# Kernel tuning notes

Measured on AMD Instinct MI355X. Metric: run time of the kernel, lower is better.

## Reference

```python
import jax, jax.numpy as jnp
import numpy as np

jax.config.update("jax_enable_x64", True)

B, T, D, L, H = 128, 256, 64, 64, 256   # batch, time steps, phys dim, latent dim, hidden width
P, DT = 4, 1.0                          # num_pred_steps, delta_t


def _mlp(x, ws, bs):
    # Conv1D(kernel_size=1) stack == per-timestep dense; relu hidden, linear output
    for i, (W, b) in enumerate(zip(ws, bs)):
        x = x @ W + b
        if i < len(ws) - 1:
            x = jax.nn.relu(x)
    return x


def setup_inputs() -> dict:
    key = jax.random.key(0)
    ks = jax.random.split(key, 9)

    def glorot(k, fi, fo):
        return jax.random.normal(k, (fi, fo), jnp.float64) * np.sqrt(2.0 / (fi + fo))

    inp = {"x": jax.random.normal(ks[0], (B, T, D), jnp.float64)}
    enc_dims = [(D, H), (H, H), (H, H), (H, L)]
    dec_dims = [(L, H), (H, H), (H, H), (H, D)]
    for i, (fi, fo) in enumerate(enc_dims):
        inp[f"enc_w{i}"] = glorot(ks[1 + i], fi, fo)
        inp[f"enc_b{i}"] = jnp.zeros((fo,), jnp.float64)
    for i, (fi, fo) in enumerate(dec_dims):
        inp[f"dec_w{i}"] = glorot(ks[5 + i], fi, fo)
        inp[f"dec_b{i}"] = jnp.zeros((fo,), jnp.float64)
    return inp


def _edmd(y, x):
    # y: [B, L, T] latent trajectories, x: [B, D, T] physical trajectories (D == L)
    y_m, y_p = y[:, :, :-1], y[:, :, 1:]
    # full_matrices=True followed by slicing to r=min(L,T-1)=L cols == reduced SVD
    U, S, Vh = jnp.linalg.svd(y_m, full_matrices=False)
    V = jnp.swapaxes(Vh, -1, -2)
    pinv = (V / S[:, None, :]) @ jnp.swapaxes(U, -1, -2)   # V @ diag(1/S) @ U^H
    K = y_p @ pinv                                         # [B, L, L]
    evals, modes = jnp.linalg.eig(K)                       # complex128
    k_evals = jnp.log(evals) / DT                          # [B, L]
    k_efuns = jnp.linalg.solve(modes, x.astype(modes.dtype))  # [B, L, T]
    xint = k_efuns[:, :, -1:]                              # [B, L, 1]

    # repeated squaring of diag eigenvalue matrix, one matvec per prediction step
    def step(e, _):
        yp = (modes @ (e[:, :, None] * xint))[..., 0]      # [B, L]
        return e * e, yp

    _, ys = jax.lax.scan(step, k_evals * k_evals, None, length=P)
    y_pred = jnp.transpose(ys, (1, 0, 2))                  # [B, P, L]
    return k_efuns, k_evals, modes, y_pred


def reference(x, enc_w0, enc_b0, enc_w1, enc_b1, enc_w2, enc_b2, enc_w3, enc_b3,
              dec_w0, dec_b0, dec_w1, dec_b1, dec_w2, dec_b2, dec_w3, dec_b3):
    ews = [enc_w0, enc_w1, enc_w2, enc_w3]
    ebs = [enc_b0, enc_b1, enc_b2, enc_b3]
    dws = [dec_w0, dec_w1, dec_w2, dec_w3]
    dbs = [dec_b0, dec_b1, dec_b2, dec_b3]

    y = _mlp(x, ews, ebs)        # [B, T, L]
    x_ae = _mlp(y, dws, dbs)     # [B, T, D]

    yt = jnp.swapaxes(y, 1, 2)   # [B, L, T]
    xt = jnp.swapaxes(x, 1, 2)   # [B, D, T]
    k_efuns, k_evals, k_modes, y_adv = _edmd(yt, xt)
    y_adv_real = jnp.real(y_adv)
    y_adv_imag = jnp.imag(y_adv)
    x_adv = _mlp(y_adv_real, dws, dbs)  # [B, P, D]
    return y, x_ae, x_adv, y_adv_real, y_adv_imag, k_evals, k_efuns, k_modes
```

## Files before the change

kernel.cpp:

```cpp
#include <hip/hip_runtime.h>
#include <hip/hip_bf16.h>

#define NB 128
#define NT 256
#define ND 64
#define NL 64
#define NH 256
#define NP 4

__device__ double g_ws[3145728];

static __device__ __forceinline__ double dlapy2_(double x, double y) {
  double ax = fabs(x), ay = fabs(y);
  double w = ax > ay ? ax : ay;
  double z = ax > ay ? ay : ax;
  if (z == 0.0) return w;
  double r = z / w;
  return w * sqrt(1.0 + r * r);
}
static __device__ __forceinline__ double sgn1_(double x) { return copysign(1.0, x); }
static __device__ __forceinline__ void cdiv_(double ar, double ai, double br, double bi,
                                             double& cr, double& ci) {
  if (fabs(br) >= fabs(bi)) {
    double r = bi / br, den = br + r * bi;
    cr = (ar + ai * r) / den;
    ci = (ai - ar * r) / den;
  } else {
    double r = br / bi, den = bi + r * br;
    cr = (ar * r + ai) / den;
    ci = (ai * r - ar) / den;
  }
}
static __device__ __forceinline__ void fwg(float* out, long long ofs, long long lim,
                                           double v) {
  if (ofs >= 0 && ofs < lim) out[ofs] = (float)v;
}
static __device__ __forceinline__ double wsum_(double v) {
  for (int o = 32; o > 0; o >>= 1) v += __shfl_xor(v, o, 64);
  return v;
}
static __device__ __forceinline__ double wmax_(double v) {
  for (int o = 32; o > 0; o >>= 1) v = fmax(v, __shfl_xor(v, o, 64));
  return v;
}

static __device__ void dlanv2_(double& a, double& b, double& c, double& d,
                               double& rt1r, double& rt1i, double& rt2r, double& rt2i,
                               double& cs, double& sn) {
  const double eps = 2.2204460492503131e-16;
  if (c == 0.0) {
    cs = 1.0; sn = 0.0;
  } else if (b == 0.0) {
    cs = 0.0; sn = 1.0;
    double temp = d; d = a; a = temp;
    b = -c; c = 0.0;
  } else if ((a - d) == 0.0 && sgn1_(b) != sgn1_(c)) {
    cs = 1.0; sn = 0.0;
  } else {
    double temp = a - d;
    double p = 0.5 * temp;
    double bcmax = fmax(fabs(b), fabs(c));
    double bcmis = fmin(fabs(b), fabs(c)) * sgn1_(b) * sgn1_(c);
    double scale = fmax(fabs(p), bcmax);
    double z = (p / scale) * p + (bcmax / scale) * bcmis;
    if (z >= 4.0 * eps) {
      z = p + copysign(sqrt(scale) * sqrt(z), p);
      a = d + z;
      d = d - (bcmax / z) * bcmis;
      double tau = dlapy2_(c, z);
      cs = z / tau; sn = c / tau;
      b = b - c; c = 0.0;
    } else {
      double sigma = b + c;
      double tau = dlapy2_(sigma, temp);
      cs = sqrt(0.5 * (1.0 + fabs(sigma) / tau));
      sn = -(p / (tau * cs)) * sgn1_(sigma);
      double aa = a * cs + b * sn, bb = -a * sn + b * cs;
      double cc = c * cs + d * sn, dd = -c * sn + d * cs;
      a = aa * cs + cc * sn; b = bb * cs + dd * sn;
      c = -aa * sn + cc * cs; d = -bb * sn + dd * cs;
      temp = 0.5 * (a + d);
      a = temp; d = temp;
      if (c != 0.0) {
        if (b != 0.0) {
          if (sgn1_(b) == sgn1_(c)) {
            double sab = sqrt(fabs(b)), sac = sqrt(fabs(c));
            double p2 = copysign(sab * sac, c);
            double tau2 = 1.0 / sqrt(fabs(b + c));
            a = temp + p2; d = temp - p2;
            b = b - c; c = 0.0;
            double cs1 = sab * tau2, sn1 = sac * tau2;
            double t0 = cs * cs1 - sn * sn1;
            sn = cs * sn1 + sn * cs1;
            cs = t0;
          }
        } else {
          b = -c; c = 0.0;
          double t0 = cs; cs = -sn; sn = t0;
        }
      }
    }
  }
  rt1r = a; rt2r = d;
  if (c == 0.0) { rt1i = 0.0; rt2i = 0.0; }
  else { rt1i = sqrt(fabs(b)) * sqrt(fabs(c)); rt2i = -rt1i; }
}

__global__ __launch_bounds__(256) void encdec_kernel(
    const float* __restrict__ x,
    const float* __restrict__ EW0, const float* __restrict__ EB0,
    const float* __restrict__ EW1, const float* __restrict__ EB1,
    const float* __restrict__ EW2, const float* __restrict__ EB2,
    const float* __restrict__ EW3, const float* __restrict__ EB3,
    const float* __restrict__ DW0, const float* __restrict__ DB0,
    const float* __restrict__ DW1, const float* __restrict__ DB1,
    const float* __restrict__ DW2, const float* __restrict__ DB2,
    const float* __restrict__ DW3, const float* __restrict__ DB3,
    float* __restrict__ out_y, double* __restrict__ y64,
    float* __restrict__ out_xae, long long lim)
{
  const int tid = threadIdx.x;
  const long long tok0 = (long long)blockIdx.x * 8;
  __shared__ double xin[8][64];
  __shared__ double h0[8][256];
  __shared__ double h1[8][256];
  for (int idx = tid; idx < 512; idx += 256) {
    int tk = idx >> 6, f2 = idx & 63;
    xin[tk][f2] = (double)x[(tok0 + tk) * 64 + f2];
  }
  __syncthreads();
  {
    int j = tid; double acc[8]; double bj = (double)EB0[j];
    for (int tk = 0; tk < 8; ++tk) acc[tk] = bj;
#pragma unroll 8
    for (int i2 = 0; i2 < 64; ++i2) {
      double w = (double)EW0[i2 * 256 + j];
      for (int tk = 0; tk < 8; ++tk) acc[tk] += xin[tk][i2] * w;
    }
    for (int tk = 0; tk < 8; ++tk) h0[tk][j] = fmax(acc[tk], 0.0);
  }
  __syncthreads();
  {
    int j = tid; double acc[8]; double bj = (double)EB1[j];
    for (int tk = 0; tk < 8; ++tk) acc[tk] = bj;
#pragma unroll 4
    for (int i2 = 0; i2 < 256; ++i2) {
      double w = (double)EW1[i2 * 256 + j];
      for (int tk = 0; tk < 8; ++tk) acc[tk] += h0[tk][i2] * w;
    }
    for (int tk = 0; tk < 8; ++tk) h1[tk][j] = fmax(acc[tk], 0.0);
  }
  __syncthreads();
  {
    int j = tid; double acc[8]; double bj = (double)EB2[j];
    for (int tk = 0; tk < 8; ++tk) acc[tk] = bj;
#pragma unroll 4
    for (int i2 = 0; i2 < 256; ++i2) {
      double w = (double)EW2[i2 * 256 + j];
      for (int tk = 0; tk < 8; ++tk) acc[tk] += h1[tk][i2] * w;
    }
    for (int tk = 0; tk < 8; ++tk) h0[tk][j] = fmax(acc[tk], 0.0);
  }
  __syncthreads();
  {
    int j = tid & 63;
    int tg = tid >> 6;
    double acc0 = (double)EB3[j], acc1 = acc0;
#pragma unroll 4
    for (int i2 = 0; i2 < 256; ++i2) {
      double w = (double)EW3[i2 * 64 + j];
      acc0 += h0[tg * 2][i2] * w;
      acc1 += h0[tg * 2 + 1][i2] * w;
    }
    for (int u = 0; u < 2; ++u) {
      int tk = tg * 2 + u;
      double a = (u == 0) ? acc0 : acc1;
      long long gl = (tok0 + tk) * 64 + j;
      xin[tk][j] = a;
      fwg(out_y, gl, lim, a);
      y64[gl] = a;
    }
  }
  __syncthreads();
  {
    int j = tid; double acc[8]; double bj = (double)DB0[j];
    for (int tk = 0; tk < 8; ++tk) acc[tk] = bj;
#pragma unroll 8
    for (int i2 = 0; i2 < 64; ++i2) {
      double w = (double)DW0[i2 * 256 + j];
      for (int tk = 0; tk < 8; ++tk) acc[tk] += xin[tk][i2] * w;
    }
    for (int tk = 0; tk < 8; ++tk) h0[tk][j] = fmax(acc[tk], 0.0);
  }
  __syncthreads();
  {
    int j = tid; double acc[8]; double bj = (double)DB1[j];
    for (int tk = 0; tk < 8; ++tk) acc[tk] = bj;
#pragma unroll 4
    for (int i2 = 0; i2 < 256; ++i2) {
      double w = (double)DW1[i2 * 256 + j];
      for (int tk = 0; tk < 8; ++tk) acc[tk] += h0[tk][i2] * w;
    }
    for (int tk = 0; tk < 8; ++tk) h1[tk][j] = fmax(acc[tk], 0.0);
  }
  __syncthreads();
  {
    int j = tid; double acc[8]; double bj = (double)DB2[j];
    for (int tk = 0; tk < 8; ++tk) acc[tk] = bj;
#pragma unroll 4
    for (int i2 = 0; i2 < 256; ++i2) {
      double w = (double)DW2[i2 * 256 + j];
      for (int tk = 0; tk < 8; ++tk) acc[tk] += h1[tk][i2] * w;
    }
    for (int tk = 0; tk < 8; ++tk) h0[tk][j] = fmax(acc[tk], 0.0);
  }
  __syncthreads();
  {
    int j = tid & 63;
    int tg = tid >> 6;
    double acc0 = (double)DB3[j], acc1 = acc0;
#pragma unroll 4
    for (int i2 = 0; i2 < 256; ++i2) {
      double w = (double)DW3[i2 * 64 + j];
      acc0 += h0[tg * 2][i2] * w;
      acc1 += h0[tg * 2 + 1][i2] * w;
    }
    fwg(out_xae, (tok0 + tg * 2) * 64 + j, lim, acc0);
    fwg(out_xae, (tok0 + tg * 2 + 1) * 64 + j, lim, acc1);
  }
}

__global__ __launch_bounds__(256) void dec4_kernel(
    const double* __restrict__ inp, long long ntok,
    const float* __restrict__ W0, const float* __restrict__ B0,
    const float* __restrict__ W1, const float* __restrict__ B1,
    const float* __restrict__ W2, const float* __restrict__ B2,
    const float* __restrict__ W3, const float* __restrict__ B3,
    float* __restrict__ outb, long long lim)
{
  const int tid = threadIdx.x;
  const long long tok0 = (long long)blockIdx.x * 8;
  __shared__ double xin[8][64];
  __shared__ double h0[8][256];
  __shared__ double h1[8][256];
  for (int idx = tid; idx < 512; idx += 256) {
    int tk = idx >> 6, f2 = idx & 63;
    long long gl = (tok0 + tk) * 64 + f2;
    xin[tk][f2] = (tok0 + tk < ntok) ? inp[gl] : 0.0;
  }
  __syncthreads();
  {
    int j = tid; double acc[8]; double bj = (double)B0[j];
    for (int tk = 0; tk < 8; ++tk) acc[tk] = bj;
#pragma unroll 8
    for (int i2 = 0; i2 < 64; ++i2) {
      double w = (double)W0[i2 * 256 + j];
      for (int tk = 0; tk < 8; ++tk) acc[tk] += xin[tk][i2] * w;
    }
    for (int tk = 0; tk < 8; ++tk) h0[tk][j] = fmax(acc[tk], 0.0);
  }
  __syncthreads();
  {
    int j = tid; double acc[8]; double bj = (double)B1[j];
    for (int tk = 0; tk < 8; ++tk) acc[tk] = bj;
#pragma unroll 4
    for (int i2 = 0; i2 < 256; ++i2) {
      double w = (double)W1[i2 * 256 + j];
      for (int tk = 0; tk < 8; ++tk) acc[tk] += h0[tk][i2] * w;
    }
    for (int tk = 0; tk < 8; ++tk) h1[tk][j] = fmax(acc[tk], 0.0);
  }
  __syncthreads();
  {
    int j = tid; double acc[8]; double bj = (double)B2[j];
    for (int tk = 0; tk < 8; ++tk) acc[tk] = bj;
#pragma unroll 4
    for (int i2 = 0; i2 < 256; ++i2) {
      double w = (double)W2[i2 * 256 + j];
      for (int tk = 0; tk < 8; ++tk) acc[tk] += h1[tk][i2] * w;
    }
    for (int tk = 0; tk < 8; ++tk) h0[tk][j] = fmax(acc[tk], 0.0);
  }
  __syncthreads();
  {
    int j = tid & 63;
    int tg = tid >> 6;
    double acc0 = (double)B3[j], acc1 = acc0;
#pragma unroll 4
    for (int i2 = 0; i2 < 256; ++i2) {
      double w = (double)W3[i2 * 64 + j];
      acc0 += h0[tg * 2][i2] * w;
      acc1 += h0[tg * 2 + 1][i2] * w;
    }
    for (int u = 0; u < 2; ++u) {
      long long tok = tok0 + tg * 2 + u;
      if (tok < ntok) fwg(outb, tok * 64 + j, lim, (u == 0) ? acc0 : acc1);
    }
  }
}

__global__ __launch_bounds__(256) void buildGA_kernel(const double* __restrict__ y64,
                                                      double* __restrict__ G,
                                                      double* __restrict__ A)
{
  int b = blockIdx.x, tid = threadIdx.x;
  __shared__ double ybuf[65][64];
  const double* yb = y64 + (size_t)b * NT * 64;
  double g[16], a[16];
  for (int s = 0; s < 16; ++s) { g[s] = 0.0; a[s] = 0.0; }
  for (int c0 = 0; c0 < 255; c0 += 64) {
    int nrow = (256 - c0 < 65) ? (256 - c0) : 65;
    for (int idx = tid; idx < nrow * 64; idx += 256) {
      int rr = idx >> 6, f2 = idx & 63;
      ybuf[rr][f2] = yb[(size_t)(c0 + rr) * 64 + f2];
    }
    __syncthreads();
    int tmax = (254 - c0 < 63) ? (254 - c0) : 63;
    for (int s = 0; s < 16; ++s) {
      int id = s * 256 + tid;
      int i2 = id >> 6, j2 = id & 63;
      double gg = g[s], aa = a[s];
      for (int tt = 0; tt <= tmax; ++tt) {
        double yj = ybuf[tt][j2];
        gg += ybuf[tt][i2] * yj;
        aa += ybuf[tt + 1][i2] * yj;
      }
      g[s] = gg; a[s] = aa;
    }
    __syncthreads();
  }
  for (int s = 0; s < 16; ++s) {
    int id = s * 256 + tid;
    G[(size_t)b * 4096 + id] = g[s];
    A[(size_t)b * 4096 + id] = a[s];
  }
}

__global__ __launch_bounds__(64) void cholsolve_kernel(const double* __restrict__ G,
                                                       const double* __restrict__ A,
                                                       double* __restrict__ Km)
{
  int b = blockIdx.x, t = threadIdx.x;
  __shared__ double C[64][65];
  __shared__ double X[64][65];
  const double* Gb = G + (size_t)b * 4096;
  const double* Ab = A + (size_t)b * 4096;
  for (int r = 0; r < 64; ++r) C[r][t] = Gb[r * 64 + t];
  for (int i2 = 0; i2 < 64; ++i2) X[i2][t] = Ab[t * 64 + i2];
  __syncthreads();
  for (int k = 0; k < 64; ++k) {
    double s = C[k][k];
    for (int m2 = 0; m2 < k; ++m2) s -= C[k][m2] * C[k][m2];
    double ckk = sqrt(fmax(s, 1e-300));
    __syncthreads();
    if (t == k) C[k][k] = ckk;
    if (t > k) {
      double v = C[t][k];
      for (int m2 = 0; m2 < k; ++m2) v -= C[t][m2] * C[k][m2];
      C[t][k] = v / ckk;
    }
    __syncthreads();
  }
  for (int i2 = 0; i2 < 64; ++i2) {
    double v = X[i2][t];
    for (int m2 = 0; m2 < i2; ++m2) v -= C[i2][m2] * X[m2][t];
    X[i2][t] = v / C[i2][i2];
  }
  for (int i2 = 63; i2 >= 0; --i2) {
    double v = X[i2][t];
    for (int m2 = i2 + 1; m2 < 64; ++m2) v -= C[m2][i2] * X[m2][t];
    X[i2][t] = v / C[i2][i2];
  }
  __syncthreads();
  for (int i2 = 0; i2 < 64; ++i2)
    Km[(size_t)b * 4096 + (size_t)t * 64 + i2] = X[i2][t];
}

__global__ __launch_bounds__(64) void eig_kernel(
    const double* __restrict__ Kmat,
    double* __restrict__ modes_re, double* __restrict__ modes_im,
    double* __restrict__ klog,
    float* __restrict__ out, long long o_kevals, long long o_kmodes,
    int cplx, long long lim)
{
  const int b = blockIdx.x;
  const int t = threadIdx.x;
  __shared__ double Hs[64][65];
  __shared__ double Zs[64][65];
  __shared__ double wr[64], wi[64], bscale[64], tau[64];
  __shared__ double xr[64], xi[64];
  double* mre = modes_re + (size_t)b * 4096;
  double* mim = modes_im + (size_t)b * 4096;

  const double ulp = 2.2204460492503131e-16;
  const double safmin = 2.2250738585072014e-308;

  for (int r = 0; r < 64; ++r) Hs[r][t] = Kmat[(size_t)b * 4096 + r * 64 + t];
  bscale[t] = 1.0;
  __syncthreads();

  {
    const double sclfac = 2.0, factor = 0.95;
    const double sfmin1 = safmin / ulp;
    const double sfmax1 = 1.0 / sfmin1;
    const double sfmin2 = sfmin1 * sclfac;
    const double sfmax2 = 1.0 / sfmin2;
    for (int sweep = 0; sweep < 64; ++sweep) {
      bool noconv = false;
      for (int i = 0; i < 64; ++i) {
        double colv = fabs(Hs[t][i]);
        double rowv = fabs(Hs[i][t]);
        double c = wsum_((t == i) ? 0.0 : colv);
        double r = wsum_((t == i) ? 0.0 : rowv);
        double ca = wmax_(colv);
        double ra = wmax_(rowv);
        if (c == 0.0 || r == 0.0) continue;
        double g = r / sclfac, f = 1.0, s = c + r;
        while (c < g) {
          if (fmax(fmax(f, c), ca) >= sfmax2 || fmin(fmin(r, g), ra) <= sfmin2) break;
          f *= sclfac; c *= sclfac; ca *= sclfac;
          r /= sclfac; g /= sclfac; ra /= sclfac;
        }
        g = c / sclfac;
        while (g >= r) {
          if (fmax(r, ra) >= sfmax2 || fmin(fmin(fmin(f, c), g), ca) <= sfmin2) break;
          f /= sclfac; c /= sclfac; g /= sclfac; ca /= sclfac;
          r *= sclfac; ra *= sclfac;
        }
        if (c + r >= factor * s) continue;
        double bsi = bscale[i];
        if (f < 1.0 && bsi < 1.0) { if (f * bsi <= sfmin1) continue; }
        if (f > 1.0 && bsi > 1.0) { if (bsi >= sfmax1 / f) continue; }
        double gi = 1.0 / f;
        Hs[i][t] *= gi;
        Hs[t][i] *= f;
        if (t == 0) bscale[i] = bsi * f;
        noconv = true;
        __syncthreads();
      }
      if (!noconv) break;
    }
    __syncthreads();
  }

  for (int i = 0; i < 62; ++i) {
    double alpha = Hs[i + 1][i];
    double contrib = (t >= i + 2) ? Hs[t][i] * Hs[t][i] : 0.0;
    double ss = wsum_(contrib);
    double taui, beta;
    if (ss == 0.0) {
      taui = 0.0; beta = alpha;
    } else {
      beta = -copysign(sqrt(alpha * alpha + ss), alpha);
      taui = (beta - alpha) / beta;
      double sc = 1.0 / (alpha - beta);
      if (t >= i + 2) Hs[t][i] *= sc;
    }
    if (t == 0) { tau[i] = taui; Hs[i + 1][i] = beta; }
    __syncthreads();
    if (taui != 0.0) {
      {
        double sum = Hs[t][i + 1];
        for (int k = i + 2; k < 64; ++k) sum += Hs[t][k] * Hs[k][i];
        sum *= taui;
        Hs[t][i + 1] -= sum;
        for (int k = i + 2; k < 64; ++k) Hs[t][k] -= sum * Hs[k][i];
      }
      __syncthreads();
      if (t >= i + 1) {
        double sum = Hs[i + 1][t];
        for (int k = i + 2; k < 64; ++k) sum += Hs[k][i] * Hs[k][t];
        sum *= taui;
        Hs[i + 1][t] -= sum;
        for (int k = i + 2; k < 64; ++k) Hs[k][t] -= sum * Hs[k][i];
      }
      __syncthreads();
    }
  }

  {
    for (int r = 0; r < 64; ++r) Zs[t][r] = (r == t) ? 1.0 : 0.0;
    for (int i = 61; i >= 0; --i) {
      double taui = tau[i];
      if (taui != 0.0) {
        double sum = Zs[t][i + 1];
        for (int k = i + 2; k < 64; ++k) sum += Hs[k][i] * Zs[t][k];
        sum *= taui;
        Zs[t][i + 1] -= sum;
        for (int k = i + 2; k < 64; ++k) Zs[t][k] -= sum * Hs[k][i];
      }
    }
  }
  __syncthreads();
  for (int r = t + 2; r < 64; ++r) Hs[r][t] = 0.0;
  __syncthreads();

  {
    const int lo = 0, hi = 63;
    const double dat1 = 0.75, dat2 = -0.4375;
    const int kexsh = 10;
    const double smlnum = safmin * (64.0 / ulp);
    int I = hi;
    int kdefl = 0;
    while (I >= lo) {
      int L = lo;
      bool done = false;
      const int itmax = 30 * 64;
      for (int its = 0; its <= itmax; ++its) {
        int k;
        {
          bool pred = false;
          int kl = t;
          if (kl > L && kl <= I) {
            double sub = fabs(Hs[kl][kl - 1]);
            if (sub <= smlnum) pred = true;
            else {
              double tst = fabs(Hs[kl - 1][kl - 1]) + fabs(Hs[kl][kl]);
              if (tst == 0.0) {
                if (kl - 2 >= lo) tst += fabs(Hs[kl - 1][kl - 2]);
                if (kl + 1 <= hi) tst += fabs(Hs[kl + 1][kl]);
              }
              if (sub <= ulp * tst) {
                double h12a = fabs(Hs[kl - 1][kl]);
                double ab = fmax(sub, h12a), ba = fmin(sub, h12a);
                double hkk = fabs(Hs[kl][kl]);
                double dif = fabs(Hs[kl - 1][kl - 1] - Hs[kl][kl]);
                double aa = fmax(hkk, dif), bb2 = fmin(hkk, dif);
                double s = aa + ab;
                if (ba * (ab / s) <= fmax(smlnum, ulp * (bb2 * (aa / s)))) pred = true;
              }
            }
          }
          unsigned long long msk = __ballot(pred);
          k = msk ? (63 - __builtin_clzll(msk)) : L;
        }
        L = k;
        if (L > lo) { if (t == 0) Hs[L][L - 1] = 0.0; }
        __syncthreads();
        if (L >= I - 1) { done = true; break; }
        kdefl++;
        double h11, h12, h21, h22;
        if (kdefl % (2 * kexsh) == 0) {
          double s = dat1 * (fabs(Hs[I][I - 1]) + fabs(Hs[I - 1][I - 2]));
          h11 = dat2 * s + Hs[I][I]; h12 = s; h21 = s; h22 = h11;
        } else if (kdefl % kexsh == 0) {
          double s = dat1 * (fabs(Hs[L + 1][L]) + fabs(Hs[L + 2][L + 1]));
          h11 = dat2 * s + Hs[L][L]; h12 = s; h21 = s; h22 = h11;
        } else {
          h11 = Hs[I - 1][I - 1]; h21 = Hs[I][I - 1];
          h12 = Hs[I - 1][I];     h22 = Hs[I][I];
        }
        double rt1r, rt1i, rt2r, rt2i;
        {
          double s = fabs(h11) + fabs(h12) + fabs(h21) + fabs(h22);
          if (s == 0.0) { rt1r = rt1i = rt2r = rt2i = 0.0; }
          else {
            double a_ = h11 / s, c_ = h21 / s, b_ = h12 / s, d_ = h22 / s;
            double tr = a_ + d_;
            double det = (a_ - d_) * (a_ - d_) * 0.25 + b_ * c_;
            if (det >= 0.0) {
              double rtdisc = sqrt(det);
              double r1 = tr * 0.5 + rtdisc;
              double r2 = tr * 0.5 - rtdisc;
              double pick = (fabs(r1 - d_) <= fabs(r2 - d_)) ? r1 : r2;
              rt1r = pick * s; rt2r = rt1r; rt1i = 0.0; rt2i = 0.0;
            } else {
              rt1r = tr * 0.5 * s; rt2r = rt1r;
              rt1i = sqrt(-det) * s; rt2i = -rt1i;
            }
          }
        }
        int m; double v0, v1, v2;
        {
          double w0 = 0.0, w1 = 0.0, w2 = 0.0;
          bool ok = false;
          int mm = t;
          if (mm >= L && mm <= I - 2) {
            double h21s = Hs[mm + 1][mm];
            double s = fabs(Hs[mm][mm] - rt2r) + fabs(rt2i) + fabs(h21s);
            h21s = Hs[mm + 1][mm] / s;
            w0 = h21s * Hs[mm][mm + 1] + (Hs[mm][mm] - rt1r) * ((Hs[mm][mm] - rt2r) / s)
                 - rt1i * (rt2i / s);
            w1 = h21s * (Hs[mm][mm] + Hs[mm + 1][mm + 1] - rt1r - rt2r);
            w2 = h21s * Hs[mm + 2][mm + 1];
            double s2 = fabs(w0) + fabs(w1) + fabs(w2);
            w0 /= s2; w1 /= s2; w2 /= s2;
            if (mm == L) ok = true;
            else ok = (fabs(Hs[mm][mm - 1]) * (fabs(w1) + fabs(w2)) <=
                       ulp * fabs(w0) *
                           (fabs(Hs[mm - 1][mm - 1]) + fabs(Hs[mm][mm]) +
                            fabs(Hs[mm + 1][mm + 1])));
          }
          unsigned long long msk = __ballot(ok);
          m = 63 - __builtin_clzll(msk);
          v0 = __shfl(w0, m); v1 = __shfl(w1, m); v2 = __shfl(w2, m);
        }
        for (int kk = m; kk <= I - 1; ++kk) {
          int nr = (3 < I - kk + 1) ? 3 : (I - kk + 1);
          double u0, u1, u2 = 0.0;
          if (kk > m) {
            u0 = Hs[kk][kk - 1]; u1 = Hs[kk + 1][kk - 1];
            u2 = (nr == 3) ? Hs[kk + 2][kk - 1] : 0.0;
          } else { u0 = v0; u1 = v1; u2 = (nr == 3) ? v2 : 0.0; }
          double t1;
          {
            double xn2 = u1 * u1 + u2 * u2;
            if (xn2 == 0.0) t1 = 0.0;
            else {
              double beta = -copysign(sqrt(u0 * u0 + xn2), u0);
              t1 = (beta - u0) / beta;
              double sc = 1.0 / (u0 - beta);
              u1 *= sc; u2 *= sc;
              u0 = beta;
            }
          }
          double t2 = t1 * u1, t3 = t1 * u2;
          if (nr == 3) {
            if (t >= kk) {
              double sum = Hs[kk][t] + u1 * Hs[kk + 1][t] + u2 * Hs[kk + 2][t];
              Hs[kk][t] -= sum * t1;
              Hs[kk + 1][t] -= sum * t2;
              Hs[kk + 2][t] -= sum * t3;
            }
          } else {
            if (t >= kk) {
              double sum = Hs[kk][t] + u1 * Hs[kk + 1][t];
              Hs[kk][t] -= sum * t1;
              Hs[kk + 1][t] -= sum * t2;
            }
          }
          if (t == 0) {
            if (kk > m) {
              Hs[kk][kk - 1] = u0;
              Hs[kk + 1][kk - 1] = 0.0;
              if (kk < I - 1) Hs[kk + 2][kk - 1] = 0.0;
            } else if (m > L) {
              Hs[kk][kk - 1] *= (1.0 - t1);
            }
          }
          __syncthreads();
          int rmax = (kk + 3 < I) ? kk + 3 : I;
          if (nr == 3) {
            if (t <= rmax) {
              double sum = Hs[t][kk] + u1 * Hs[t][kk + 1] + u2 * Hs[t][kk + 2];
              Hs[t][kk] -= sum * t1;
              Hs[t][kk + 1] -= sum * t2;
              Hs[t][kk + 2] -= sum * t3;
            }
            {
              double z0 = Zs[kk][t], z1 = Zs[kk + 1][t], z2 = Zs[kk + 2][t];
              double sum = z0 + u1 * z1 + u2 * z2;
              Zs[kk][t] = z0 - sum * t1;
              Zs[kk + 1][t] = z1 - sum * t2;
              Zs[kk + 2][t] = z2 - sum * t3;
            }
          } else {
            if (t <= rmax) {
              double sum = Hs[t][kk] + u1 * Hs[t][kk + 1];
              Hs[t][kk] -= sum * t1;
              Hs[t][kk + 1] -= sum * t2;
            }
            {
              double z0 = Zs[kk][t], z1 = Zs[kk + 1][t];
              double sum = z0 + u1 * z1;
              Zs[kk][t] = z0 - sum * t1;
              Zs[kk + 1][t] = z1 - sum * t2;
            }
          }
          __syncthreads();
        }
      }
      if (!done) {
        __syncthreads();
        if (t == 0) {
          for (int r = lo; r <= I; ++r) { wr[r] = Hs[r][r]; wi[r] = 0.0; }
        }
        __syncthreads();
        I = lo - 1;
        kdefl = 0;
        continue;
      }
      if (L == I) {
        if (t == 0) { wr[I] = Hs[I][I]; wi[I] = 0.0; }
        __syncthreads();
      } else {
        double a_ = Hs[I - 1][I - 1], b_ = Hs[I - 1][I];
        double c_ = Hs[I][I - 1],     d_ = Hs[I][I];
        double r1r, r1i, r2r, r2i, cs, sn;
        dlanv2_(a_, b_, c_, d_, r1r, r1i, r2r, r2i, cs, sn);
        __syncthreads();
        if (t == 0) {
          Hs[I - 1][I - 1] = a_; Hs[I - 1][I] = b_;
          Hs[I][I - 1] = c_;     Hs[I][I] = d_;
          wr[I - 1] = r1r; wi[I - 1] = r1i;
          wr[I] = r2r;     wi[I] = r2i;
        }
        __syncthreads();
        if (t > I) {
          double x = Hs[I - 1][t], y = Hs[I][t];
          Hs[I - 1][t] = cs * x + sn * y;
          Hs[I][t] = cs * y - sn * x;
        }
        if (t < I - 1) {
          double x = Hs[t][I - 1], y = Hs[t][I];
          Hs[t][I - 1] = cs * x + sn * y;
          Hs[t][I] = cs * y - sn * x;
        }
        {
          double x = Zs[I - 1][t], y = Zs[I][t];
          Zs[I - 1][t] = cs * x + sn * y;
          Zs[I][t] = cs * y - sn * x;
        }
        __syncthreads();
      }
      kdefl = 0;
      I = L - 1;
    }
  }
  __syncthreads();

  const double smln = safmin * (64.0 / ulp);
  int ki = 63;
  while (ki >= 0) {
    bool pair = (ki > 0) && (Hs[ki][ki - 1] != 0.0);
    if (!pair) {
      double lam = wr[ki];
      double smin = fmax(ulp * fabs(lam), smln);
      xr[t] = (t < ki) ? -Hs[t][ki] : ((t == ki) ? 1.0 : 0.0);
      __syncthreads();
      int j = ki - 1;
      while (j >= 0) {
        bool blk2 = (j > 0) && (Hs[j][j - 1] != 0.0);
        if (!blk2) {
          double den = Hs[j][j] - lam;
          if (fabs(den) < smin) den = smin;
          double xj = xr[j] / den;
          if (t == j) xr[j] = xj;
          else if (t < j) xr[t] -= xj * Hs[t][j];
          __syncthreads();
          j -= 1;
        } else {
          double t11 = Hs[j - 1][j - 1] - lam, t12 = Hs[j - 1][j];
          double t21 = Hs[j][j - 1], t22 = Hs[j][j] - lam;
          double det = t11 * t22 - t12 * t21;
          if (fabs(det) < smin * smin) det = copysign(smin * smin, (det == 0.0) ? 1.0 : det);
          double b1 = xr[j - 1], b2 = xr[j];
          double x1 = (b1 * t22 - t12 * b2) / det;
          double x2 = (t11 * b2 - t21 * b1) / det;
          if (t == j - 1) xr[j - 1] = x1;
          else if (t == j) xr[j] = x2;
          else if (t < j - 1) xr[t] -= x1 * Hs[t][j - 1] + x2 * Hs[t][j];
          __syncthreads();
          j -= 2;
        }
      }
      double acc = 0.0;
      for (int k2 = 0; k2 <= ki; ++k2) acc += Zs[k2][t] * xr[k2];
      acc *= bscale[t];
      double nn = wsum_(acc * acc);
      double scl = 1.0 / sqrt(nn);
      mre[t * 64 + ki] = acc * scl;
      mim[t * 64 + ki] = 0.0;
      ki -= 1;
    } else {
      double wre = Hs[ki][ki];
      double wim = sqrt(fabs(Hs[ki][ki - 1])) * sqrt(fabs(Hs[ki - 1][ki]));
      double smin = fmax(ulp * (fabs(wre) + wim), smln);
      double seed_r_km1, seed_i_k;
      if (fabs(Hs[ki - 1][ki]) >= fabs(Hs[ki][ki - 1])) {
        seed_r_km1 = 1.0;
        seed_i_k = wim / Hs[ki - 1][ki];
      } else {
        seed_r_km1 = -wim / Hs[ki][ki - 1];
        seed_i_k = 1.0;
      }
      if (t < ki - 1) {
        xr[t] = -seed_r_km1 * Hs[t][ki - 1];
        xi[t] = -seed_i_k * Hs[t][ki];
      } else if (t == ki - 1) { xr[t] = seed_r_km1; xi[t] = 0.0; }
      else if (t == ki) { xr[t] = 0.0; xi[t] = seed_i_k; }
      else { xr[t] = 0.0; xi[t] = 0.0; }
      __syncthreads();
      int j = ki - 2;
      while (j >= 0) {
        bool blk2 = (j > 0) && (Hs[j][j - 1] != 0.0);
        if (!blk2) {
          double dr = Hs[j][j] - wre, di = -wim;
          if (fabs(dr) + fabs(di) < smin) { dr = smin; di = 0.0; }
          double xjr, xji;
          cdiv_(xr[j], xi[j], dr, di, xjr, xji);
          if (t == j) { xr[j] = xjr; xi[j] = xji; }
          else if (t < j) {
            xr[t] -= xjr * Hs[t][j];
            xi[t] -= xji * Hs[t][j];
          }
          __syncthreads();
          j -= 1;
        } else {
          double t11 = Hs[j - 1][j - 1] - wre, t12 = Hs[j - 1][j];
          double t21 = Hs[j][j - 1], t22 = Hs[j][j] - wre;
          double detr = t11 * t22 - wim * wim - t12 * t21;
          double deti = -wim * (t11 + t22);
          double b1r = xr[j - 1], b1i = xi[j - 1];
          double b2r = xr[j], b2i = xi[j];
          double n1r = b1r * t22 + b1i * wim - t12 * b2r;
          double n1i = b1i * t22 - b1r * wim - t12 * b2i;
          double n2r = t11 * b2r + b2i * wim - t21 * b1r;
          double n2i = t11 * b2i - b2r * wim - t21 * b1i;
          double x1r, x1i, x2r, x2i;
          cdiv_(n1r, n1i, detr, deti, x1r, x1i);
          cdiv_(n2r, n2i, detr, deti, x2r, x2i);
          if (t == j - 1) { xr[t] = x1r; xi[t] = x1i; }
          else if (t == j) { xr[t] = x2r; xi[t] = x2i; }
          else if (t < j - 1) {
            xr[t] -= x1r * Hs[t][j - 1] + x2r * Hs[t][j];
            xi[t] -= x1i * Hs[t][j - 1] + x2i * Hs[t][j];
          }
          __syncthreads();
          j -= 2;
        }
      }
      double ar = 0.0, ai = 0.0;
      for (int k2 = 0; k2 <= ki; ++k2) {
        double z = Zs[k2][t];
        ar += z * xr[k2];
        ai += z * xi[k2];
      }
      ar *= bscale[t]; ai *= bscale[t];
      double n2a = wsum_(ar * ar), n2b = wsum_(ai * ai);
      double scl = 1.0 / dlapy2_(sqrt(n2a), sqrt(n2b));
      double vr0 = ar * scl, vi0 = ai * scl;
      double mm = vr0 * vr0 + vi0 * vi0;
      double mmax = wmax_(mm);
      unsigned long long msk = __ballot(mm == mmax);
      int kmx = __ffsll((unsigned long long)msk) - 1;
      double f = __shfl(vr0, kmx), g = __shfl(vi0, kmx);
      double cs_, sn_;
      if (g == 0.0) { cs_ = 1.0; sn_ = 0.0; }
      else if (f == 0.0) { cs_ = 0.0; sn_ = sgn1_(g); }
      else {
        double dd = sqrt(f * f + g * g);
        double sg = sgn1_(f);
        cs_ = fabs(f) / dd;
        sn_ = sg * g / dd;
      }
      double nr0 = cs_ * vr0 + sn_ * vi0;
      double ni0 = cs_ * vi0 - sn_ * vr0;
      if (t == kmx) ni0 = 0.0;
      mre[t * 64 + (ki - 1)] = nr0;
      mim[t * 64 + (ki - 1)] = ni0;
      mre[t * 64 + ki] = nr0;
      mim[t * 64 + ki] = -ni0;
      ki -= 2;
    }
  }

  {
    double er = wr[t], ei = wi[t];
    double lr = log(dlapy2_(er, ei));
    double li = atan2(ei, er);
    klog[(size_t)b * 128 + 2 * t] = lr;
    klog[(size_t)b * 128 + 2 * t + 1] = li;
    if (cplx) {
      fwg(out, o_kevals + ((long long)b * 64 + t) * 2, lim, lr);
      fwg(out, o_kevals + ((long long)b * 64 + t) * 2 + 1, lim, li);
    } else {
      fwg(out, o_kevals + (long long)b * 64 + t, lim, lr);
    }
  }
  for (int k2 = 0; k2 < 64; ++k2) {
    long long idx = ((long long)b * 64 + t) * 64 + k2;
    if (cplx) {
      fwg(out, o_kmodes + idx * 2, lim, mre[t * 64 + k2]);
      fwg(out, o_kmodes + idx * 2 + 1, lim, mim[t * 64 + k2]);
    } else {
      fwg(out, o_kmodes + idx, lim, mre[t * 64 + k2]);
    }
  }
}

__global__ __launch_bounds__(64) void lu_kernel(
    const double* __restrict__ mre, const double* __restrict__ mim,
    double* __restrict__ lure, double* __restrict__ luim, int* __restrict__ piv)
{
  int b = blockIdx.x, t = threadIdx.x;
  __shared__ double Lre[64][65], Lim[64][65];
  for (int r = 0; r < 64; ++r) {
    Lre[r][t] = mre[(size_t)b * 4096 + r * 64 + t];
    Lim[r][t] = mim[(size_t)b * 4096 + r * 64 + t];
  }
  __syncthreads();
  for (int k = 0; k < 64; ++k) {
    double mval = (t >= k) ? (fabs(Lre[t][k]) + fabs(Lim[t][k])) : -1.0;
    double mmax = wmax_(mval);
    unsigned long long msk = __ballot(mval == mmax);
    int p = __ffsll(msk) - 1;
    if (t == 0) piv[b * 64 + k] = p;
    if (p != k) {
      double a0 = Lre[k][t], a1 = Lim[k][t];
      Lre[k][t] = Lre[p][t]; Lim[k][t] = Lim[p][t];
      Lre[p][t] = a0; Lim[p][t] = a1;
    }
    __syncthreads();
    double pr = Lre[k][k], pi = Lim[k][k];
    if (t > k) {
      double lr, li;
      cdiv_(Lre[t][k], Lim[t][k], pr, pi, lr, li);
      Lre[t][k] = lr; Lim[t][k] = li;
      for (int c = k + 1; c < 64; ++c) {
        double ur = Lre[k][c], ui = Lim[k][c];
        Lre[t][c] -= lr * ur - li * ui;
        Lim[t][c] -= lr * ui + li * ur;
      }
    }
    __syncthreads();
  }
  for (int r = 0; r < 64; ++r) {
    lure[(size_t)b * 4096 + r * 64 + t] = Lre[r][t];
    luim[(size_t)b * 4096 + r * 64 + t] = Lim[r][t];
  }
}

__global__ __launch_bounds__(64) void lusolve_kernel(
    const double* __restrict__ lure, const double* __restrict__ luim,
    const int* __restrict__ piv, const float* __restrict__ x_in,
    float* __restrict__ out, long long o_kefuns, int cplx,
    double* __restrict__ xint, long long lim)
{
  int b = blockIdx.x >> 2;
  int chunk = blockIdx.x & 3;
  int t = threadIdx.x;
  int tglob = chunk * 64 + t;
  __shared__ double br_[64][64], bi_[64][64];
  const double* Lr = lure + (size_t)b * 4096;
  const double* Li = luim + (size_t)b * 4096;
  for (int i2 = 0; i2 < 64; ++i2) {
    br_[i2][t] = (double)x_in[((size_t)b * 256 + tglob) * 64 + i2];
    bi_[i2][t] = 0.0;
  }
  const int* pv = piv + b * 64;
  for (int k = 0; k < 64; ++k) {
    int p = pv[k];
    if (p != k) {
      double a0 = br_[k][t], a1 = bi_[k][t];
      br_[k][t] = br_[p][t]; bi_[k][t] = bi_[p][t];
      br_[p][t] = a0; bi_[p][t] = a1;
    }
  }
  for (int k = 0; k < 63; ++k) {
    double bkr = br_[k][t], bki = bi_[k][t];
    for (int i2 = k + 1; i2 < 64; ++i2) {
      double lr = Lr[i2 * 64 + k], li = Li[i2 * 64 + k];
      br_[i2][t] -= lr * bkr - li * bki;
      bi_[i2][t] -= lr * bki + li * bkr;
    }
  }
  for (int k = 63; k >= 0; --k) {
    double xr0, xi0;
    cdiv_(br_[k][t], bi_[k][t], Lr[k * 64 + k], Li[k * 64 + k], xr0, xi0);
    br_[k][t] = xr0; bi_[k][t] = xi0;
    for (int i2 = 0; i2 < k; ++i2) {
      double ur = Lr[i2 * 64 + k], ui = Li[i2 * 64 + k];
      br_[i2][t] -= ur * xr0 - ui * xi0;
      bi_[i2][t] -= ur * xi0 + ui * xr0;
    }
  }
  for (int i2 = 0; i2 < 64; ++i2) {
    long long idx = ((long long)b * 64 + i2) * 256 + tglob;
    if (cplx) {
      fwg(out, o_kefuns + idx * 2, lim, br_[i2][t]);
      fwg(out, o_kefuns + idx * 2 + 1, lim, bi_[i2][t]);
    } else {
      fwg(out, o_kefuns + idx, lim, br_[i2][t]);
    }
  }
  if (tglob == 255) {
    for (int i2 = 0; i2 < 64; ++i2) {
      xint[(size_t)b * 128 + 2 * i2] = br_[i2][t];
      xint[(size_t)b * 128 + 2 * i2 + 1] = bi_[i2][t];
    }
  }
}

__global__ __launch_bounds__(64) void ypred_kernel(
    const double* __restrict__ klog, const double* __restrict__ xint,
    const double* __restrict__ mre, const double* __restrict__ mim,
    float* __restrict__ out, long long o_yadvr, long long o_yadvi,
    double* __restrict__ yadv64, long long lim)
{
  int b = blockIdx.x, t = threadIdx.x;
  __shared__ double er[64], ei[64], wxr[64], wxi[64];
  double kr = klog[(size_t)b * 128 + 2 * t], kiv = klog[(size_t)b * 128 + 2 * t + 1];
  er[t] = kr * kr - kiv * kiv;
  ei[t] = 2.0 * kr * kiv;
  double xr0 = xint[(size_t)b * 128 + 2 * t], xi0 = xint[(size_t)b * 128 + 2 * t + 1];
  __syncthreads();
  for (int p = 0; p < 4; ++p) {
    wxr[t] = er[t] * xr0 - ei[t] * xi0;
    wxi[t] = er[t] * xi0 + ei[t] * xr0;
    __syncthreads();
    double ar = 0.0, ai = 0.0;
    const double* mr = mre + (size_t)b * 4096 + (size_t)t * 64;
    const double* mi = mim + (size_t)b * 4096 + (size_t)t * 64;
    for (int k = 0; k < 64; ++k) {
      double wr0 = wxr[k], wi0 = wxi[k];
      ar += mr[k] * wr0 - mi[k] * wi0;
      ai += mr[k] * wi0 + mi[k] * wr0;
    }
    long long idx = ((long long)b * 4 + p) * 64 + t;
    fwg(out, o_yadvr + idx, lim, ar);
    fwg(out, o_yadvi + idx, lim, ai);
    yadv64[idx] = ar;
    double e2r = er[t] * er[t] - ei[t] * ei[t];
    double e2i = 2.0 * er[t] * ei[t];
    __syncthreads();
    er[t] = e2r; ei[t] = e2i;
    __syncthreads();
  }
}

extern "C" void kernel_launch(void* const* d_in, const int* in_sizes, int n_in,
                              void* d_out, int out_size, void* d_ws, size_t ws_size,
                              hipStream_t stream) {
  (void)in_sizes; (void)n_in; (void)d_ws; (void)ws_size;
  const float* x = (const float*)d_in[0];
  const float* ew0 = (const float*)d_in[1];  const float* eb0 = (const float*)d_in[2];
  const float* ew1 = (const float*)d_in[3];  const float* eb1 = (const float*)d_in[4];
  const float* ew2 = (const float*)d_in[5];  const float* eb2 = (const float*)d_in[6];
  const float* ew3 = (const float*)d_in[7];  const float* eb3 = (const float*)d_in[8];
  const float* dw0 = (const float*)d_in[9];  const float* db0 = (const float*)d_in[10];
  const float* dw1 = (const float*)d_in[11]; const float* db1 = (const float*)d_in[12];
  const float* dw2 = (const float*)d_in[13]; const float* db2 = (const float*)d_in[14];
  const float* dw3 = (const float*)d_in[15]; const float* db3 = (const float*)d_in[16];
  float* out = (float*)d_out;
  const long long lim = (long long)out_size;

  void* wsp = nullptr;
  hipGetSymbolAddress(&wsp, HIP_SYMBOL(g_ws));
  char* ws = (char*)wsp;
  double* y64  = (double*)(ws + 0);
  double* G    = (double*)(ws + 16777216);
  double* A    = (double*)(ws + 20971520);
  double* Km   = (double*)(ws + 0);
  double* mre  = (double*)(ws + 8388608);
  double* mim  = (double*)(ws + 12582912);
  double* klog = (double*)(ws + 16777216);
  double* lure = (double*)(ws + 17825792);
  double* luim = (double*)(ws + 0);
  int*    piv  = (int*)   (ws + 22020096);
  double* xint = (double*)(ws + 22052864);
  double* yadv = (double*)(ws + 22183936);

  const long long n_y = 2097152, n_s = 32768;
  int cplx = (out_size > 8000000) ? 1 : 0;
  long long o_y = 0, o_xae = n_y, o_xadv = 2 * n_y;
  long long o_yadvr = o_xadv + n_s, o_yadvi = o_yadvr + n_s;
  long long o_kevals = o_yadvi + n_s;
  long long o_kefuns, o_kmodes;
  if (cplx) { o_kefuns = o_kevals + 2 * 8192;  o_kmodes = o_kefuns + 2 * 2097152; }
  else      { o_kefuns = o_kevals + 8192;      o_kmodes = o_kefuns + 2097152; }

  encdec_kernel<<<4096, 256, 0, stream>>>(x,
      ew0, eb0, ew1, eb1, ew2, eb2, ew3, eb3,
      dw0, db0, dw1, db1, dw2, db2, dw3, db3,
      out + o_y, y64, out + o_xae, lim);
  buildGA_kernel<<<128, 256, 0, stream>>>(y64, G, A);
  cholsolve_kernel<<<128, 64, 0, stream>>>(G, A, Km);
  eig_kernel<<<128, 64, 0, stream>>>(Km, mre, mim, klog, out, o_kevals, o_kmodes,
                                     cplx, lim);
  lu_kernel<<<128, 64, 0, stream>>>(mre, mim, lure, luim, piv);
  lusolve_kernel<<<512, 64, 0, stream>>>(lure, luim, piv, x, out, o_kefuns, cplx,
                                         xint, lim);
  ypred_kernel<<<128, 64, 0, stream>>>(klog, xint, mre, mim, out, o_yadvr, o_yadvi,
                                       yadv, lim);
  dec4_kernel<<<64, 256, 0, stream>>>(yadv, 512,
      dw0, db0, dw1, db1, dw2, db2, dw3, db3, out + o_xadv, lim);
}
```

Before: 5.114 ms.

## Move autoencoder decoder into eig kernel blocks in fp32 to overlap serial eig

Splits the encoder/decoder kernel so that the x_ae decoder MLP runs as 4096 extra blocks appended to the eigen-decomposition launch. Those blocks can fill the GPU while the 128 serial eig blocks run. The decoder now computes in float32 instead of double, with 64-thread blocks each handling 4 output columns. The workspace is enlarged and re-laid out so y64 is not overwritten before the decoder blocks read it. The trade-off is lower precision for x_ae and possible scheduling contention with the long-running eig blocks.

```diff
diff --git a/kernel.cpp b/kernel.cpp
--- a/kernel.cpp
+++ b/kernel.cpp
@@ -8,7 +8,7 @@
 #define NH 256
 #define NP 4
 
-__device__ double g_ws[3145728];
+__device__ double g_ws[3932160];
 
 static __device__ __forceinline__ double dlapy2_(double x, double y) {
   double ax = fabs(x), ay = fabs(y);
@@ -106,18 +106,13 @@
   else { rt1i = sqrt(fabs(b)) * sqrt(fabs(c)); rt2i = -rt1i; }
 }
 
-__global__ __launch_bounds__(256) void encdec_kernel(
+__global__ __launch_bounds__(256) void enc_kernel(
     const float* __restrict__ x,
     const float* __restrict__ EW0, const float* __restrict__ EB0,
     const float* __restrict__ EW1, const float* __restrict__ EB1,
     const float* __restrict__ EW2, const float* __restrict__ EB2,
     const float* __restrict__ EW3, const float* __restrict__ EB3,
-    const float* __restrict__ DW0, const float* __restrict__ DB0,
-    const float* __restrict__ DW1, const float* __restrict__ DB1,
-    const float* __restrict__ DW2, const float* __restrict__ DB2,
-    const float* __restrict__ DW3, const float* __restrict__ DB3,
-    float* __restrict__ out_y, double* __restrict__ y64,
-    float* __restrict__ out_xae, long long lim)
+    float* __restrict__ out_y, double* __restrict__ y64, long long lim)
 {
   const int tid = threadIdx.x;
   const long long tok0 = (long long)blockIdx.x * 8;
@@ -176,57 +171,9 @@
       int tk = tg * 2 + u;
       double a = (u == 0) ? acc0 : acc1;
       long long gl = (tok0 + tk) * 64 + j;
-      xin[tk][j] = a;
       fwg(out_y, gl, lim, a);
       y64[gl] = a;
     }
-  }
-  __syncthreads();
-  {
-    int j = tid; double acc[8]; double bj = (double)DB0[j];
-    for (int tk = 0; tk < 8; ++tk) acc[tk] = bj;
-#pragma unroll 8
-    for (int i2 = 0; i2 < 64; ++i2) {
-      double w = (double)DW0[i2 * 256 + j];
-      for (int tk = 0; tk < 8; ++tk) acc[tk] += xin[tk][i2] * w;
-    }
-    for (int tk = 0; tk < 8; ++tk) h0[tk][j] = fmax(acc[tk], 0.0);
-  }
-  __syncthreads();
-  {
-    int j = tid; double acc[8]; double bj = (double)DB1[j];
-    for (int tk = 0; tk < 8; ++tk) acc[tk] = bj;
-#pragma unroll 4
-    for (int i2 = 0; i2 < 256; ++i2) {
-      double w = (double)DW1[i2 * 256 + j];
-      for (int tk = 0; tk < 8; ++tk) acc[tk] += h0[tk][i2] * w;
-    }
-    for (int tk = 0; tk < 8; ++tk) h1[tk][j] = fmax(acc[tk], 0.0);
-  }
-  __syncthreads();
-  {
-    int j = tid; double acc[8]; double bj = (double)DB2[j];
-    for (int tk = 0; tk < 8; ++tk) acc[tk] = bj;
-#pragma unroll 4
-    for (int i2 = 0; i2 < 256; ++i2) {
-      double w = (double)DW2[i2 * 256 + j];
-      for (int tk = 0; tk < 8; ++tk) acc[tk] += h1[tk][i2] * w;
-    }
-    for (int tk = 0; tk < 8; ++tk) h0[tk][j] = fmax(acc[tk], 0.0);
-  }
-  __syncthreads();
-  {
-    int j = tid & 63;
-    int tg = tid >> 6;
-    double acc0 = (double)DB3[j], acc1 = acc0;
-#pragma unroll 4
-    for (int i2 = 0; i2 < 256; ++i2) {
-      double w = (double)DW3[i2 * 64 + j];
-      acc0 += h0[tg * 2][i2] * w;
-      acc1 += h0[tg * 2 + 1][i2] * w;
-    }
-    fwg(out_xae, (tok0 + tg * 2) * 64 + j, lim, acc0);
-    fwg(out_xae, (tok0 + tg * 2 + 1) * 64 + j, lim, acc1);
   }
 }
 
@@ -376,19 +323,104 @@
     Km[(size_t)b * 4096 + (size_t)t * 64 + i2] = X[i2][t];
 }
 
-__global__ __launch_bounds__(64) void eig_kernel(
+__global__ __launch_bounds__(64) void eig_dec_kernel(
     const double* __restrict__ Kmat,
     double* __restrict__ modes_re, double* __restrict__ modes_im,
     double* __restrict__ klog,
     float* __restrict__ out, long long o_kevals, long long o_kmodes,
-    int cplx, long long lim)
+    int cplx, long long lim,
+    const double* __restrict__ y64,
+    const float* __restrict__ DW0, const float* __restrict__ DB0,
+    const float* __restrict__ DW1, const float* __restrict__ DB1,
+    const float* __restrict__ DW2, const float* __restrict__ DB2,
+    const float* __restrict__ DW3, const float* __restrict__ DB3,
+    float* __restrict__ out_xae)
 {
+  const int t = threadIdx.x;
+  __shared__ __align__(16) double smem[8704];
+
+  if (blockIdx.x >= NB) {
+    const int blk = blockIdx.x - NB;
+    const long long tok0 = (long long)blk * 8;
+    float (*fx)[64] = (float (*)[64])(smem);
+    float (*fh0)[256] = (float (*)[256])(smem + 256);
+    float (*fh1)[256] = (float (*)[256])(smem + 1280);
+    for (int idx = t; idx < 512; idx += 64) {
+      int tk = idx >> 6, f2 = idx & 63;
+      fx[tk][f2] = (float)y64[(tok0 + tk) * 64 + f2];
+    }
+    __syncthreads();
+    float acc[4][8];
+    for (int s = 0; s < 4; ++s) {
+      float bj = DB0[t + 64 * s];
+      for (int tk = 0; tk < 8; ++tk) acc[s][tk] = bj;
+    }
+#pragma unroll 4
+    for (int i = 0; i < 64; ++i) {
+      float xv[8];
+      for (int tk = 0; tk < 8; ++tk) xv[tk] = fx[tk][i];
+      for (int s = 0; s < 4; ++s) {
+        float w = DW0[i * 256 + t + 64 * s];
+        for (int tk = 0; tk < 8; ++tk) acc[s][tk] += xv[tk] * w;
+      }
+    }
+    for (int s = 0; s < 4; ++s)
+      for (int tk = 0; tk < 8; ++tk) fh0[tk][t + 64 * s] = fmaxf(acc[s][tk], 0.0f);
+    __syncthreads();
+    for (int s = 0; s < 4; ++s) {
+      float bj = DB1[t + 64 * s];
+      for (int tk = 0; tk < 8; ++tk) acc[s][tk] = bj;
+    }
+#pragma unroll 2
+    for (int i = 0; i < 256; ++i) {
+      float xv[8];
+      for (int tk = 0; tk < 8; ++tk) xv[tk] = fh0[tk][i];
+      for (int s = 0; s < 4; ++s) {
+        float w = DW1[i * 256 + t + 64 * s];
+        for (int tk = 0; tk < 8; ++tk) acc[s][tk] += xv[tk] * w;
+      }
+    }
+    for (int s = 0; s < 4; ++s)
+      for (int tk = 0; tk < 8; ++tk) fh1[tk][t + 64 * s] = fmaxf(acc[s][tk], 0.0f);
+    __syncthreads();
+    for (int s = 0; s < 4; ++s) {
+      float bj = DB2[t + 64 * s];
+      for (int tk = 0; tk < 8; ++tk) acc[s][tk] = bj;
+    }
+#pragma unroll 2
+    for (int i = 0; i < 256; ++i) {
+      float xv[8];
+      for (int tk = 0; tk < 8; ++tk) xv[tk] = fh1[tk][i];
+      for (int s = 0; s < 4; ++s) {
+        float w = DW2[i * 256 + t + 64 * s];
+        for (int tk = 0; tk < 8; ++tk) acc[s][tk] += xv[tk] * w;
+      }
+    }
+    for (int s = 0; s < 4; ++s)
+      for (int tk = 0; tk < 8; ++tk) fh0[tk][t + 64 * s] = fmaxf(acc[s][tk], 0.0f);
+    __syncthreads();
+    float a4[8];
+    float bj3 = DB3[t];
+    for (int tk = 0; tk < 8; ++tk) a4[tk] = bj3;
+#pragma unroll 2
+    for (int i = 0; i < 256; ++i) {
+      float w = DW3[i * 64 + t];
+      for (int tk = 0; tk < 8; ++tk) a4[tk] += fh0[tk][i] * w;
+    }
+    for (int tk = 0; tk < 8; ++tk)
+      fwg(out_xae, (tok0 + tk) * 64 + t, lim, (double)a4[tk]);
+    return;
+  }
+
   const int b = blockIdx.x;
-  const int t = threadIdx.x;
-  __shared__ double Hs[64][65];
-  __shared__ double Zs[64][65];
-  __shared__ double wr[64], wi[64], bscale[64], tau[64];
-  __shared__ double xr[64], xi[64];
+  double (*Hs)[65] = (double (*)[65])smem;
+  double (*Zs)[65] = (double (*)[65])(smem + 4160);
+  double* wr = smem + 8320;
+  double* wi = wr + 64;
+  double* bscale = wi + 64;
+  double* tau = bscale + 64;
+  double* xr = tau + 64;
+  double* xi = xr + 64;
   double* mre = modes_re + (size_t)b * 4096;
   double* mim = modes_im + (size_t)b * 4096;
 
@@ -1041,15 +1073,15 @@
   double* y64  = (double*)(ws + 0);
   double* G    = (double*)(ws + 16777216);
   double* A    = (double*)(ws + 20971520);
-  double* Km   = (double*)(ws + 0);
-  double* mre  = (double*)(ws + 8388608);
-  double* mim  = (double*)(ws + 12582912);
-  double* klog = (double*)(ws + 16777216);
-  double* lure = (double*)(ws + 17825792);
+  double* Km   = (double*)(ws + 25165824);
+  double* mre  = (double*)(ws + 16777216);
+  double* mim  = (double*)(ws + 20971520);
+  double* lure = (double*)(ws + 25165824);
   double* luim = (double*)(ws + 0);
-  int*    piv  = (int*)   (ws + 22020096);
-  double* xint = (double*)(ws + 22052864);
-  double* yadv = (double*)(ws + 22183936);
+  double* klog = (double*)(ws + 29360128);
+  double* xint = (double*)(ws + 29491200);
+  double* yadv = (double*)(ws + 29622272);
+  int*    piv  = (int*)   (ws + 29884416);
 
   const long long n_y = 2097152, n_s = 32768;
   int cplx = (out_size > 8000000) ? 1 : 0;
@@ -1060,14 +1092,13 @@
   if (cplx) { o_kefuns = o_kevals + 2 * 8192;  o_kmodes = o_kefuns + 2 * 2097152; }
   else      { o_kefuns = o_kevals + 8192;      o_kmodes = o_kefuns + 2097152; }
 
-  encdec_kernel<<<4096, 256, 0, stream>>>(x,
-      ew0, eb0, ew1, eb1, ew2, eb2, ew3, eb3,
-      dw0, db0, dw1, db1, dw2, db2, dw3, db3,
-      out + o_y, y64, out + o_xae, lim);
+  enc_kernel<<<4096, 256, 0, stream>>>(x,
+      ew0, eb0, ew1, eb1, ew2, eb2, ew3, eb3, out + o_y, y64, lim);
   buildGA_kernel<<<128, 256, 0, stream>>>(y64, G, A);
   cholsolve_kernel<<<128, 64, 0, stream>>>(G, A, Km);
-  eig_kernel<<<128, 64, 0, stream>>>(Km, mre, mim, klog, out, o_kevals, o_kmodes,
-                                     cplx, lim);
+  eig_dec_kernel<<<128 + 4096, 64, 0, stream>>>(Km, mre, mim, klog,
+      out, o_kevals, o_kmodes, cplx, lim,
+      y64, dw0, db0, dw1, db1, dw2, db2, dw3, db3, out + o_xae);
   lu_kernel<<<128, 64, 0, stream>>>(mre, mim, lure, luim, piv);
   lusolve_kernel<<<512, 64, 0, stream>>>(lure, luim, piv, x, out, o_kefuns, cplx,
                                          xint, lim);
```

Measured after the change: 4.878 ms. -4.6%, faster.
